# Performance work log

Hardware: AMD Instinct MI355X
Metric: run time of the kernel (lower is better)

The kernel has to match this reference:

```python
import jax, jax.numpy as jnp
import numpy as np

N, E = 50000, 1600000
H, C = 4, 32            # heads, out_channels per head (hidden_dim // heads)
HID, LAT = 128, 32
NEG_SLOPE = 0.2


def setup_inputs() -> dict:
    key = jax.random.key(0)
    ks = jax.random.split(key, 16)
    g = lambda k, shape, fan: jax.random.normal(k, shape, jnp.float32) * (1.0 / np.sqrt(fan))
    return {
        "x": jax.random.normal(ks[0], (N, 3), jnp.float32),
        "edge_index": jax.random.randint(ks[1], (2, E), 0, N, jnp.int64),
        "edge_attr": jax.random.normal(ks[2], (E, 7), jnp.float32),
        # GATConv params
        "W_gat": g(ks[3], (3, H * C), 3),          # lin (shared src/dst)
        "att_src": g(ks[4], (H, C), C),
        "att_dst": g(ks[5], (H, C), C),
        "W_edge": g(ks[6], (7, H * C), 7),         # lin_edge
        "att_edge": g(ks[7], (H, C), C),
        "bias_gat": jnp.zeros((H * C,), jnp.float32),
        # GCNEncoder MLP params
        "W1": g(ks[8], (HID, HID), HID),
        "b1": jnp.zeros((HID,), jnp.float32),
        "prelu_a": jnp.float32(0.25),
        "W2": g(ks[9], (HID, LAT), HID),
        "b2": jnp.zeros((LAT,), jnp.float32),
    }


def _gat_encoder(x, edge_index, edge_attr, W_gat, att_src, att_dst, W_edge,
                 att_edge, bias_gat, W1, b1, prelu_a, W2, b2):
    src, dst = edge_index[0], edge_index[1]
    n = x.shape[0]

    # add self-loops; self-loop edge_attr = mean of incoming edge_attr (PyG fill_value='mean')
    deg = jax.ops.segment_sum(jnp.ones_like(dst, jnp.float32), dst, num_segments=n)
    ea_mean = jax.ops.segment_sum(edge_attr, dst, num_segments=n) / jnp.clip(deg, 1.0)[:, None]
    loops = jnp.arange(n, dtype=src.dtype)
    src_f = jnp.concatenate([src, loops])
    dst_f = jnp.concatenate([dst, loops])
    ea_f = jnp.concatenate([edge_attr, ea_mean], axis=0)

    xp = (x @ W_gat).reshape(n, H, C)                      # [N,H,C]
    a_src = jnp.einsum('nhc,hc->nh', xp, att_src)          # [N,H]
    a_dst = jnp.einsum('nhc,hc->nh', xp, att_dst)
    ep = (ea_f @ W_edge).reshape(-1, H, C)                 # [E',H,C]
    a_edge = jnp.einsum('ehc,hc->eh', ep, att_edge)

    alpha = jax.nn.leaky_relu(a_src[src_f] + a_dst[dst_f] + a_edge, NEG_SLOPE)  # [E',H]
    m = jax.ops.segment_max(alpha, dst_f, num_segments=n)
    ealpha = jnp.exp(alpha - m[dst_f])
    denom = jax.ops.segment_sum(ealpha, dst_f, num_segments=n)
    alpha = ealpha / denom[dst_f]

    msg = xp[src_f] * alpha[:, :, None]                    # [E',H,C]
    out = jax.ops.segment_sum(msg, dst_f, num_segments=n)  # [N,H,C]
    h = jax.nn.elu(out.reshape(n, H * C) + bias_gat)

    h1 = h @ W1 + b1
    h1 = jnp.where(h1 > 0, h1, prelu_a * h1)               # PReLU
    return h1 @ W2 + b2


def reference(x, edge_index, edge_attr, W_gat, att_src, att_dst, W_edge,
              att_edge, bias_gat, W1, b1, prelu_a, W2, b2):
    return _gat_encoder(x, edge_index, edge_attr, W_gat, att_src, att_dst,
                        W_edge, att_edge, bias_gat, W1, b1, prelu_a, W2, b2)
```

## Files before the change

kernel.cpp:

```cpp
#include <hip/hip_runtime.h>
#include <cstdint>

#define N_NODES 50000
#define N_EDGES 1600000
#define NH 4
#define CC 32
#define HC 128
#define LAT 32
#define NEG_SLOPE 0.2f

#define NB_HIST 250
#define CH_E    6400
#define NB_NODE 25
#define NB_PRE  (NB_HIST + NB_NODE + 3)

#define NBUCK 196
#define P1_T  512
#define P1_EPB (P1_T * 4)
#define P1_BLOCKS ((N_EDGES + P1_EPB - 1) / P1_EPB)
#define CAP  8960

typedef uint32_t u32x4 __attribute__((ext_vector_type(4)));
typedef __bf16   bf16x8 __attribute__((ext_vector_type(8)));
typedef float    f32x4 __attribute__((ext_vector_type(4)));

__device__ __forceinline__ float bflo(uint32_t u) {
    union { uint32_t i; float f; } c; c.i = u << 16; return c.f;
}
__device__ __forceinline__ float bfhi(uint32_t u) {
    union { uint32_t i; float f; } c; c.i = u & 0xFFFF0000u; return c.f;
}
__device__ __forceinline__ uint32_t f2bf(float f) {
    union { float f; uint32_t i; } c; c.f = f;
    return (c.i + 0x7FFFu + ((c.i >> 16) & 1u)) >> 16;
}
__device__ __forceinline__ uint32_t pack2(float a, float b) {
    return f2bf(a) | (f2bf(b) << 16);
}
__device__ __forceinline__ float bpermf(int byteIdx, float v) {
    return __int_as_float(__builtin_amdgcn_ds_bpermute(byteIdx, __float_as_int(v)));
}
__device__ __forceinline__ uint32_t f2e4m3(float x) {
    uint32_t u = __float_as_uint(x);
    uint32_t s = u >> 31;
    uint32_t mag = u & 0x7fffffffu;
    mag += 0x7ffffu + ((mag >> 20) & 1u);
    uint32_t e = mag >> 23;
    if (e < 121u) return s << 7;
    uint32_t code = ((e - 120u) << 3) | ((mag >> 20) & 7u);
    if (code > 0x7Eu) code = 0x7Eu;
    return (s << 7) | code;
}
__device__ __forceinline__ float e4m32f(uint32_t b) {
    uint32_t e = (b >> 3) & 15u;
    if (e == 0u) return 0.f;
    return __uint_as_float(((b >> 7) << 31) | ((e + 120u) << 23) | ((b & 7u) << 20));
}


__global__ __launch_bounds__(256) void k_pre(const float* __restrict__ x,
                                             const int* __restrict__ ei,
                                             const float* __restrict__ W_gat,
                                             const float* __restrict__ att_src,
                                             const float* __restrict__ att_dst,
                                             const float* __restrict__ W_edge,
                                             const float* __restrict__ att_edge,
                                             const float* __restrict__ W1,
                                             const float* __restrict__ W2,
                                             uint16_t* __restrict__ hist,
                                             float4* __restrict__ a_src,
                                             float4* __restrict__ a_dst,
                                             float* __restrict__ v,
                                             uint16_t* __restrict__ W1T_hi,
                                             uint16_t* __restrict__ W1T_lo,
                                             uint16_t* __restrict__ W2T_hi,
                                             uint16_t* __restrict__ W2T_lo) {
    __shared__ uint32_t lh[12500];
    int bid = blockIdx.x, t = threadIdx.x;
    if (bid < NB_HIST) {
        int b = bid;
        int base = b * CH_E;
        uint32_t* orow = (uint32_t*)(hist + (size_t)b * N_NODES);
        #pragma unroll 1
        for (int p = 0; p < 2; ++p) {
            for (int i = t; i < 12500; i += 256) lh[i] = 0;
            __syncthreads();
            int lo = p * 25000;
            #pragma unroll 1
            for (int it = 0; it < CH_E / 256; ++it) {
                int dst = ei[N_EDGES + base + it * 256 + t];
                int r = dst - lo;
                if (r >= 0 && r < 25000)
                    atomicAdd(&lh[r >> 1], 1u << ((r & 1) * 16));
            }
            __syncthreads();
            for (int i = t; i < 12500; i += 256)
                orow[p * 12500 + i] = lh[i];
            __syncthreads();
        }
    } else if (bid < NB_HIST + NB_NODE) {
        __shared__ float us[12], ud[12];
        if (t < 12) {
            int i = t >> 2, h = t & 3;
            float s = 0.f;
            #pragma unroll
            for (int c = 0; c < 32; ++c)
                s += W_gat[i * 128 + h * 32 + c] * att_src[h * 32 + c];
            us[t] = s;
        } else if (t < 24) {
            int q = t - 12; int i = q >> 2, h = q & 3;
            float s = 0.f;
            #pragma unroll
            for (int c = 0; c < 32; ++c)
                s += W_gat[i * 128 + h * 32 + c] * att_dst[h * 32 + c];
            ud[q] = s;
        }
        __syncthreads();
        int base = (bid - NB_HIST) * 2048;
        #pragma unroll 1
        for (int i = 0; i < 8; ++i) {
            int n = base + i * 256 + t;
            if (n >= N_NODES) break;
            float x0 = x[n * 3 + 0], x1 = x[n * 3 + 1], x2 = x[n * 3 + 2];
            float s[4], d[4];
            #pragma unroll
            for (int h = 0; h < 4; ++h) {
                s[h] = x0 * us[h] + x1 * us[4 + h] + x2 * us[8 + h];
                d[h] = x0 * ud[h] + x1 * ud[4 + h] + x2 * ud[8 + h];
            }
            a_src[n] = make_float4(s[0], s[1], s[2], s[3]);
            a_dst[n] = make_float4(d[0], d[1], d[2], d[3]);
        }
    } else if (bid == NB_HIST + NB_NODE) {
        if (t < 28) {
            int d = t >> 2, h = t & 3;
            float s = 0.f;
            #pragma unroll
            for (int c = 0; c < 32; ++c)
                s += W_edge[d * 128 + h * 32 + c] * att_edge[h * 32 + c];
            v[t] = s;
        }
    } else if (bid == NB_HIST + NB_NODE + 1) {
        #pragma unroll 4
        for (int i = 0; i < 64; ++i) {
            int idx = i * 256 + t;
            int n = idx >> 7, k = idx & 127;
            float vv = W1[k * 128 + n];
            uint32_t hi = f2bf(vv);
            uint32_t lo = f2bf(vv - bflo(hi));
            W1T_hi[idx] = (uint16_t)hi;
            W1T_lo[idx] = (uint16_t)lo;
        }
    } else {
        #pragma unroll 4
        for (int i = 0; i < 16; ++i) {
            int idx = i * 256 + t;
            int j = idx >> 7, k = idx & 127;
            float vv = W2[k * 32 + j];
            uint32_t hi = f2bf(vv);
            uint32_t lo = f2bf(vv - bflo(hi));
            W2T_hi[idx] = (uint16_t)hi;
            W2T_lo[idx] = (uint16_t)lo;
        }
    }
}

__global__ __launch_bounds__(256) void k_red(const uint16_t* __restrict__ hist,
                                             int* __restrict__ cnt,
                                             int* __restrict__ bsum) {
    __shared__ int red[256];
    int t = threadIdx.x;
    int i = blockIdx.x * 256 + t;
    int run = 0;
    if (i < N_NODES) {
        int r[10];
        #pragma unroll
        for (int j = 0; j < 10; ++j) r[j] = 0;
        size_t off = i;
        #pragma unroll 1
        for (int b = 0; b < 25; ++b) {
            #pragma unroll
            for (int j = 0; j < 10; ++j)
                r[j] += hist[off + (size_t)j * N_NODES];
            off += (size_t)10 * N_NODES;
        }
        #pragma unroll
        for (int j = 1; j < 10; ++j) r[0] += r[j];
        run = r[0];
        cnt[i] = run;
    }
    red[t] = run;
    __syncthreads();
    #pragma unroll
    for (int s = 128; s > 0; s >>= 1) {
        if (t < s) red[t] += red[t + s];
        __syncthreads();
    }
    if (t == 0) bsum[blockIdx.x] = red[0];
}

__global__ __launch_bounds__(256) void k_scanb(const int* __restrict__ bsum,
                                               int* __restrict__ bbase) {
    __shared__ int sh[256];
    int t = threadIdx.x;
    int vv = (t < NBUCK) ? bsum[t] : 0;
    sh[t] = vv;
    __syncthreads();
    #pragma unroll
    for (int off = 1; off < 256; off <<= 1) {
        int xv = (t >= off) ? sh[t - off] : 0;
        __syncthreads();
        sh[t] += xv;
        __syncthreads();
    }
    if (t < NBUCK) bbase[t] = sh[t] - vv;
    if (t == 255) bbase[NBUCK] = sh[255];
}

__global__ __launch_bounds__(256) void k_local(const int* __restrict__ cnt,
                                               const int* __restrict__ bbase,
                                               int* __restrict__ rowptr,
                                               int* __restrict__ bcur) {
    __shared__ int sh[256];
    int b = blockIdx.x, t = threadIdx.x;
    int i = b * 256 + t;
    int vv = (i < N_NODES) ? cnt[i] : 0;
    sh[t] = vv;
    __syncthreads();
    #pragma unroll
    for (int off = 1; off < 256; off <<= 1) {
        int xv = (t >= off) ? sh[t - off] : 0;
        __syncthreads();
        sh[t] += xv;
        __syncthreads();
    }
    int base = bbase[b];
    if (i < N_NODES) rowptr[i] = base + sh[t] - vv;
    if (t == 0) bcur[b] = base;
    if (b == 0 && t == 0) rowptr[N_NODES] = bbase[NBUCK];
}

__global__ __launch_bounds__(512) void k_scat1(const int* __restrict__ ei,
                                               const float* __restrict__ edge_attr,
                                               const float* __restrict__ v,
                                               const float4* __restrict__ a_src,
                                               int* __restrict__ bcur,
                                               uint4* __restrict__ stg) {
    __shared__ int bh[NBUCK];
    __shared__ int bg[NBUCK];
    __shared__ int bl[NBUCK];
    __shared__ int bo[NBUCK];
    __shared__ int sct[256];
    __shared__ u32x4 lrec[P1_EPB];
    __shared__ int gaddr[P1_EPB];
    int t = threadIdx.x;
    float vsr[28];
    #pragma unroll
    for (int i = 0; i < 28; ++i) vsr[i] = v[i];

    for (int i = t; i < NBUCK; i += P1_T) bh[i] = 0;
    __syncthreads();

    int e0 = blockIdx.x * P1_EPB + t * 4;
    bool act = (e0 < N_EDGES);
    int dst[4];
    uint4 rec[4];
    if (act) {
        int4 s4 = *(const int4*)&ei[e0];
        int4 d4 = *(const int4*)&ei[N_EDGES + e0];
        int srcv[4] = {s4.x, s4.y, s4.z, s4.w};
        dst[0] = d4.x; dst[1] = d4.y; dst[2] = d4.z; dst[3] = d4.w;

        float4 as4[4];
        #pragma unroll
        for (int q = 0; q < 4; ++q)
            as4[q] = a_src[srcv[q]];

        const float4* ea4 = (const float4*)&edge_attr[e0 * 7];
        float ea[28];
        #pragma unroll
        for (int i = 0; i < 7; ++i) {
            float4 vv = ea4[i];
            ea[i * 4 + 0] = vv.x; ea[i * 4 + 1] = vv.y;
            ea[i * 4 + 2] = vv.z; ea[i * 4 + 3] = vv.w;
        }

        #pragma unroll
        for (int q = 0; q < 4; ++q) {
            float asv[4] = {as4[q].x, as4[q].y, as4[q].z, as4[q].w};
            float comb[4];
            uint32_t ae8 = 0;
            #pragma unroll
            for (int h = 0; h < 4; ++h) {
                float aeh = 0.f;
                #pragma unroll
                for (int d = 0; d < 7; ++d) aeh += ea[q * 7 + d] * vsr[d * 4 + h];
                ae8 |= f2e4m3(aeh) << (h * 8);
                comb[h] = aeh + asv[h];
            }
            rec[q] = make_uint4(pack2(comb[0], comb[1]), pack2(comb[2], comb[3]),
                                (uint32_t)srcv[q] | ((uint32_t)(dst[q] & 255) << 16),
                                ae8);
            atomicAdd(&bh[dst[q] >> 8], 1);
        }
    }
    __syncthreads();
    int hv = 0;
    if (t < 256) { hv = (t < NBUCK) ? bh[t] : 0; sct[t] = hv; }
    __syncthreads();
    #pragma unroll
    for (int off = 1; off < 256; off <<= 1) {
        int xv = 0;
        if (t < 256 && t >= off) xv = sct[t - off];
        __syncthreads();
        if (t < 256) sct[t] += xv;
        __syncthreads();
    }
    if (t < NBUCK) {
        bo[t] = sct[t] - hv;
        bg[t] = hv ? atomicAdd(&bcur[t], hv) : 0;
        bl[t] = 0;
    }
    __syncthreads();
    if (act) {
        #pragma unroll
        for (int q = 0; q < 4; ++q) {
            int bk = dst[q] >> 8;
            int off = atomicAdd(&bl[bk], 1);
            int slot = bo[bk] + off;
            lrec[slot] = (u32x4){rec[q].x, rec[q].y, rec[q].z, rec[q].w};
            gaddr[slot] = bg[bk] + off;
        }
    }
    __syncthreads();
    int total = sct[255];
    for (int s = t; s < total; s += P1_T) {
        u32x4 r = lrec[s];
        stg[gaddr[s]] = make_uint4(r.x, r.y, r.z, r.w);
    }
}

__global__ __launch_bounds__(1024) void k_scat2g(const int* __restrict__ rowptr,
                                                 const int* __restrict__ bbase,
                                                 const uint4* __restrict__ stg,
                                                 const float* __restrict__ x,
                                                 const float* __restrict__ a_src,
                                                 const float* __restrict__ a_dst,
                                                 const float* __restrict__ W_gat,
                                                 const float* __restrict__ bias_gat,
                                                 float2* __restrict__ h_buf) {
    __shared__ int rp[257];
    __shared__ int lcnt[256];
    __shared__ u32x4 lrec[CAP];
    int b = blockIdx.x, t = threadIdx.x;
    int n0 = b << 8;
    int nn = min(256, N_NODES - n0);
    int base = bbase[b];
    for (int i = t; i <= nn; i += 1024) rp[i] = rowptr[n0 + i] - base;
    __syncthreads();
    for (int i = t; i < nn; i += 1024) lcnt[i] = rp[i + 1] - rp[i];
    __syncthreads();
    int total = rp[nn];

    for (int e = t; e < total; e += 1024) {
        uint4 r = stg[base + e];
        int dl = (int)((r.z >> 16) & 0xFFu);
        int c = atomicSub(&lcnt[dl], 1);
        int slot = rp[dl] + c - 1;
        if (slot < CAP) lrec[slot] = (u32x4){r.x, r.y, r.z, r.w};
    }
    __syncthreads();

    int wv = t >> 6, l = t & 63;
    int h = l & 3;
    int slot = l >> 2;
    int c0 = 2 * l;
    float w00 = W_gat[c0],       w01 = W_gat[c0 + 1];
    float w10 = W_gat[128 + c0], w11 = W_gat[128 + c0 + 1];
    float w20 = W_gat[256 + c0], w21 = W_gat[256 + c0 + 1];
    float2 bia = ((const float2*)bias_gat)[l];

    #pragma unroll 1
    for (int j = 0; j < 16; ++j) {
        int i = wv * 16 + j;
        if (i >= nn) break;
        int n = n0 + i;
        int start = rp[i], end = rp[i + 1];
        int deg = end - start;
        float ad_n = a_dst[n * 4 + h];
        float as_n = a_src[n * 4 + h];
        float sx0 = 0.f, sx1 = 0.f, sx2 = 0.f, den = 0.f, aes = 0.f;

        for (int p0 = start; p0 < end; p0 += 16) {
            int e = p0 + slot;
            float w = 0.f, ae = 0.f;
            int src = n;
            if (e < end) {
                u32x4 rc = lrec[e];
                uint32_t aw = (h < 2) ? rc.x : rc.y;
                float comb = (h & 1) ? bfhi(aw) : bflo(aw);
                ae = e4m32f((rc.w >> (h * 8)) & 0xffu);
                src = (int)(rc.z & 0xFFFFu);
                float al = comb + ad_n;
                al = al > 0.f ? al : NEG_SLOPE * al;
                w = __expf(al);
            }
            const float* xr = x + src * 3;
            sx0 += w * xr[0];
            sx1 += w * xr[1];
            sx2 += w * xr[2];
            den += w;
            aes += ae;
        }

        #pragma unroll
        for (int m = 4; m <= 32; m <<= 1) {
            sx0 += __shfl_xor(sx0, m);
            sx1 += __shfl_xor(sx1, m);
            sx2 += __shfl_xor(sx2, m);
            den += __shfl_xor(den, m);
            aes += __shfl_xor(aes, m);
        }

        float xn0 = x[n * 3], xn1 = x[n * 3 + 1], xn2 = x[n * 3 + 2];
        float invd = (deg > 0) ? (1.0f / (float)deg) : 1.0f;
        float alS = as_n + ad_n + aes * invd;
        alS = alS > 0.f ? alS : NEG_SLOPE * alS;
        float wS = __expf(alS);
        sx0 += wS * xn0; sx1 += wS * xn1; sx2 += wS * xn2;
        den += wS;

        int sb = (l >> 4) << 2;
        float t0 = bpermf(sb, sx0);
        float t1 = bpermf(sb, sx1);
        float t2 = bpermf(sb, sx2);
        float td = bpermf(sb, den);

        float r = 1.0f / td;
        float o0 = (t0 * w00 + t1 * w10 + t2 * w20) * r + bia.x;
        float o1 = (t0 * w01 + t1 * w11 + t2 * w21) * r + bia.y;
        o0 = o0 > 0.f ? o0 : (__expf(o0) - 1.0f);
        o1 = o1 > 0.f ? o1 : (__expf(o1) - 1.0f);
        h_buf[(size_t)n * 64 + l] = make_float2(o0, o1);
    }
}

__global__ __launch_bounds__(256) void k_mlp(const float* __restrict__ h_buf,
                                             const uint16_t* __restrict__ W1T_hi,
                                             const uint16_t* __restrict__ W1T_lo,
                                             const uint16_t* __restrict__ W2T_hi,
                                             const uint16_t* __restrict__ W2T_lo,
                                             const float* __restrict__ b1,
                                             const float* __restrict__ prelu_a,
                                             const float* __restrict__ b2,
                                             float* __restrict__ out) {
    __shared__ uint16_t hHi[32 * 136];
    __shared__ uint16_t hLo[32 * 136];
    __shared__ uint16_t h1Hi[32 * 136];
    __shared__ uint16_t h1Lo[32 * 136];
    int t = threadIdx.x;
    int nb = blockIdx.x * 32;

    const float4* hb4 = (const float4*)(h_buf + (size_t)nb * 128);
    #pragma unroll
    for (int i = 0; i < 4; ++i) {
        int idx = i * 256 + t;
        int row = idx >> 5, c4 = idx & 31;
        float4 v = make_float4(0.f, 0.f, 0.f, 0.f);
        if (nb + row < N_NODES) v = hb4[idx];
        float xs[4] = {v.x, v.y, v.z, v.w};
        uint32_t hi[4], lo[4];
        #pragma unroll
        for (int j = 0; j < 4; ++j) {
            hi[j] = f2bf(xs[j]);
            lo[j] = f2bf(xs[j] - bflo(hi[j]));
        }
        uint32_t bo = row * 272 + c4 * 8;
        *(uint2*)((char*)hHi + bo) = make_uint2(hi[0] | (hi[1] << 16), hi[2] | (hi[3] << 16));
        *(uint2*)((char*)hLo + bo) = make_uint2(lo[0] | (lo[1] << 16), lo[2] | (lo[3] << 16));
    }
    __syncthreads();

    int w = t >> 6, l = t & 63;
    int lr = l & 15, lg = l >> 4;
    float bb0 = b1[(2 * w) * 16 + lr];
    float bb1 = b1[(2 * w + 1) * 16 + lr];
    f32x4 acc[2][2];
    #pragma unroll
    for (int rt = 0; rt < 2; ++rt) {
        acc[rt][0] = (f32x4){bb0, bb0, bb0, bb0};
        acc[rt][1] = (f32x4){bb1, bb1, bb1, bb1};
    }
    #pragma unroll
    for (int s = 0; s < 4; ++s) {
        int koff = s * 64 + lg * 16;
        bf16x8 a_hi[2], a_lo[2], b_hi[2], b_lo[2];
        #pragma unroll
        for (int rt = 0; rt < 2; ++rt) {
            int ro = (rt * 16 + lr) * 272 + koff;
            a_hi[rt] = *(const bf16x8*)((const char*)hHi + ro);
            a_lo[rt] = *(const bf16x8*)((const char*)hLo + ro);
        }
        #pragma unroll
        for (int c = 0; c < 2; ++c) {
            int go = ((2 * w + c) * 16 + lr) * 256 + koff;
            b_hi[c] = *(const bf16x8*)((const char*)W1T_hi + go);
            b_lo[c] = *(const bf16x8*)((const char*)W1T_lo + go);
        }
        #pragma unroll
        for (int rt = 0; rt < 2; ++rt)
            #pragma unroll
            for (int c = 0; c < 2; ++c) {
                acc[rt][c] = __builtin_amdgcn_mfma_f32_16x16x32_bf16(a_hi[rt], b_hi[c], acc[rt][c], 0, 0, 0);
                acc[rt][c] = __builtin_amdgcn_mfma_f32_16x16x32_bf16(a_hi[rt], b_lo[c], acc[rt][c], 0, 0, 0);
                acc[rt][c] = __builtin_amdgcn_mfma_f32_16x16x32_bf16(a_lo[rt], b_hi[c], acc[rt][c], 0, 0, 0);
            }
    }
    float pa = prelu_a[0];
    #pragma unroll
    for (int rt = 0; rt < 2; ++rt)
        #pragma unroll
        for (int c = 0; c < 2; ++c) {
            int n = (2 * w + c) * 16 + lr;
            #pragma unroll
            for (int r = 0; r < 4; ++r) {
                float vv = acc[rt][c][r];
                vv = vv > 0.f ? vv : pa * vv;
                uint32_t hi = f2bf(vv);
                uint32_t lo = f2bf(vv - bflo(hi));
                int m = rt * 16 + lg * 4 + r;
                uint32_t bo = m * 272 + n * 2;
                *(uint16_t*)((char*)h1Hi + bo) = (uint16_t)hi;
                *(uint16_t*)((char*)h1Lo + bo) = (uint16_t)lo;
            }
        }
    __syncthreads();
    int rt2 = w & 1, ct2 = w >> 1;
    float bb2 = b2[ct2 * 16 + lr];
    f32x4 acc2 = (f32x4){bb2, bb2, bb2, bb2};
    #pragma unroll
    for (int s = 0; s < 4; ++s) {
        int koff = s * 64 + lg * 16;
        int ro = (rt2 * 16 + lr) * 272 + koff;
        bf16x8 a_hi = *(const bf16x8*)((const char*)h1Hi + ro);
        bf16x8 a_lo = *(const bf16x8*)((const char*)h1Lo + ro);
        int go = (ct2 * 16 + lr) * 256 + koff;
        bf16x8 w2h = *(const bf16x8*)((const char*)W2T_hi + go);
        bf16x8 w2l = *(const bf16x8*)((const char*)W2T_lo + go);
        acc2 = __builtin_amdgcn_mfma_f32_16x16x32_bf16(a_hi, w2h, acc2, 0, 0, 0);
        acc2 = __builtin_amdgcn_mfma_f32_16x16x32_bf16(a_hi, w2l, acc2, 0, 0, 0);
        acc2 = __builtin_amdgcn_mfma_f32_16x16x32_bf16(a_lo, w2h, acc2, 0, 0, 0);
    }
    #pragma unroll
    for (int r = 0; r < 4; ++r) {
        int m = rt2 * 16 + lg * 4 + r;
        if (nb + m < N_NODES)
            out[(size_t)(nb + m) * 32 + ct2 * 16 + lr] = acc2[r];
    }
}


extern "C" void kernel_launch(void* const* d_in, const int* in_sizes, int n_in,
                              void* d_out, int out_size, void* d_ws, size_t ws_size,
                              hipStream_t stream) {
    const float* x        = (const float*)d_in[0];
    const int*   ei       = (const int*)d_in[1];
    const float* edge_attr= (const float*)d_in[2];
    const float* W_gat    = (const float*)d_in[3];
    const float* att_src  = (const float*)d_in[4];
    const float* att_dst  = (const float*)d_in[5];
    const float* W_edge   = (const float*)d_in[6];
    const float* att_edge = (const float*)d_in[7];
    const float* bias_gat = (const float*)d_in[8];
    const float* W1       = (const float*)d_in[9];
    const float* b1       = (const float*)d_in[10];
    const float* prelu_a  = (const float*)d_in[11];
    const float* W2       = (const float*)d_in[12];
    const float* b2       = (const float*)d_in[13];
    float*       out      = (float*)d_out;

    char* base = (char*)d_ws;
    size_t off = 0;
    auto alloc = [&](size_t bytes) -> void* {
        void* p = base + off;
        off = (off + bytes + 255) & ~(size_t)255;
        return p;
    };
    int*      cnt     = (int*)     alloc((size_t)N_NODES * 4);
    int*      rowptr  = (int*)     alloc((size_t)(N_NODES + 1) * 4);
    int*      bcur    = (int*)     alloc((size_t)NBUCK * 4);
    int*      bsum    = (int*)     alloc((size_t)NBUCK * 4);
    int*      bbase   = (int*)     alloc((size_t)(NBUCK + 1) * 4);
    float*    v       = (float*)   alloc(32 * 4);
    uint16_t* W1T_hi  = (uint16_t*)alloc((size_t)128 * 128 * 2);
    uint16_t* W1T_lo  = (uint16_t*)alloc((size_t)128 * 128 * 2);
    uint16_t* W2T_hi  = (uint16_t*)alloc((size_t)32 * 128 * 2);
    uint16_t* W2T_lo  = (uint16_t*)alloc((size_t)32 * 128 * 2);
    float*    a_src   = (float*)   alloc((size_t)N_NODES * 4 * 4);
    float*    a_dst   = (float*)   alloc((size_t)N_NODES * 4 * 4);
    float*    h_buf   = (float*)   alloc((size_t)N_NODES * 128 * 4);
    size_t stg_bytes  = (size_t)N_EDGES * 16;
    size_t hist_bytes = (size_t)NB_HIST * N_NODES * 2;
    void* stg_region  = alloc(stg_bytes > hist_bytes ? stg_bytes : hist_bytes);
    uint16_t* hist    = (uint16_t*)stg_region;
    uint4*    stg     = (uint4*)stg_region;

    k_pre   <<<NB_PRE, 256, 0, stream>>>(x, ei, W_gat, att_src, att_dst,
                                         W_edge, att_edge, W1, W2, hist,
                                         (float4*)a_src, (float4*)a_dst, v,
                                         W1T_hi, W1T_lo, W2T_hi, W2T_lo);
    k_red   <<<NBUCK, 256, 0, stream>>>(hist, cnt, bsum);
    k_scanb <<<1, 256, 0, stream>>>(bsum, bbase);
    k_local <<<NBUCK, 256, 0, stream>>>(cnt, bbase, rowptr, bcur);
    k_scat1 <<<P1_BLOCKS, P1_T, 0, stream>>>(
        ei, edge_attr, v, (const float4*)a_src, bcur, stg);
    k_scat2g<<<NBUCK, 1024, 0, stream>>>(
        rowptr, bbase, stg, x, a_src, a_dst, W_gat, bias_gat, (float2*)h_buf);
    k_mlp   <<<(N_NODES + 31) / 32, 256, 0, stream>>>(
        h_buf, W1T_hi, W1T_lo, W2T_hi, W2T_lo, b1, prelu_a, b2, out);
}
```

Before: 243.8 us.

## Replace per-block LDS histograms with global atomic degree counting

Degree counting previously built per-block shared-memory histograms (packed 16-bit counters over two passes), wrote 250 partial rows to global memory, and reduced them in a separate kernel. Now each edge does a global atomicAdd into a zeroed count array, and the reduce kernel only computes block sums. This removes the large partial-histogram write and read (about 25 MB) and the two-pass LDS work. In exchange it adds 1.6M contended global atomics and an extra zeroing kernel launch.

```diff
diff --git a/kernel.cpp b/kernel.cpp
--- a/kernel.cpp
+++ b/kernel.cpp
@@ -9,10 +9,10 @@
 #define LAT 32
 #define NEG_SLOPE 0.2f
 
-#define NB_HIST 250
+#define NB_CNT  250
 #define CH_E    6400
 #define NB_NODE 25
-#define NB_PRE  (NB_HIST + NB_NODE + 3)
+#define NB_PRE  (NB_CNT + NB_NODE + 3)
 
 #define NBUCK 196
 #define P1_T  512
@@ -58,6 +58,11 @@
 }
 
 
+__global__ __launch_bounds__(1024) void k_zero(int* __restrict__ cnt) {
+    int i = blockIdx.x * 1024 + threadIdx.x;
+    if (i < N_NODES) cnt[i] = 0;
+}
+
 __global__ __launch_bounds__(256) void k_pre(const float* __restrict__ x,
                                              const int* __restrict__ ei,
                                              const float* __restrict__ W_gat,
@@ -67,7 +72,7 @@
                                              const float* __restrict__ att_edge,
                                              const float* __restrict__ W1,
                                              const float* __restrict__ W2,
-                                             uint16_t* __restrict__ hist,
+                                             int* __restrict__ cnt,
                                              float4* __restrict__ a_src,
                                              float4* __restrict__ a_dst,
                                              float* __restrict__ v,
@@ -75,30 +80,15 @@
                                              uint16_t* __restrict__ W1T_lo,
                                              uint16_t* __restrict__ W2T_hi,
                                              uint16_t* __restrict__ W2T_lo) {
-    __shared__ uint32_t lh[12500];
     int bid = blockIdx.x, t = threadIdx.x;
-    if (bid < NB_HIST) {
-        int b = bid;
-        int base = b * CH_E;
-        uint32_t* orow = (uint32_t*)(hist + (size_t)b * N_NODES);
+    if (bid < NB_CNT) {
+        int base = bid * CH_E;
         #pragma unroll 1
-        for (int p = 0; p < 2; ++p) {
-            for (int i = t; i < 12500; i += 256) lh[i] = 0;
-            __syncthreads();
-            int lo = p * 25000;
-            #pragma unroll 1
-            for (int it = 0; it < CH_E / 256; ++it) {
-                int dst = ei[N_EDGES + base + it * 256 + t];
-                int r = dst - lo;
-                if (r >= 0 && r < 25000)
-                    atomicAdd(&lh[r >> 1], 1u << ((r & 1) * 16));
-            }
-            __syncthreads();
-            for (int i = t; i < 12500; i += 256)
-                orow[p * 12500 + i] = lh[i];
-            __syncthreads();
-        }
-    } else if (bid < NB_HIST + NB_NODE) {
+        for (int it = 0; it < CH_E / 256; ++it) {
+            int dst = ei[N_EDGES + base + it * 256 + t];
+            atomicAdd(&cnt[dst], 1);
+        }
+    } else if (bid < NB_CNT + NB_NODE) {
         __shared__ float us[12], ud[12];
         if (t < 12) {
             int i = t >> 2, h = t & 3;
@@ -116,7 +106,7 @@
             ud[q] = s;
         }
         __syncthreads();
-        int base = (bid - NB_HIST) * 2048;
+        int base = (bid - NB_CNT) * 2048;
         #pragma unroll 1
         for (int i = 0; i < 8; ++i) {
             int n = base + i * 256 + t;
@@ -131,7 +121,7 @@
             a_src[n] = make_float4(s[0], s[1], s[2], s[3]);
             a_dst[n] = make_float4(d[0], d[1], d[2], d[3]);
         }
-    } else if (bid == NB_HIST + NB_NODE) {
+    } else if (bid == NB_CNT + NB_NODE) {
         if (t < 28) {
             int d = t >> 2, h = t & 3;
             float s = 0.f;
@@ -140,7 +130,7 @@
                 s += W_edge[d * 128 + h * 32 + c] * att_edge[h * 32 + c];
             v[t] = s;
         }
-    } else if (bid == NB_HIST + NB_NODE + 1) {
+    } else if (bid == NB_CNT + NB_NODE + 1) {
         #pragma unroll 4
         for (int i = 0; i < 64; ++i) {
             int idx = i * 256 + t;
@@ -165,31 +155,12 @@
     }
 }
 
-__global__ __launch_bounds__(256) void k_red(const uint16_t* __restrict__ hist,
-                                             int* __restrict__ cnt,
-                                             int* __restrict__ bsum) {
+__global__ __launch_bounds__(256) void k_bsum(const int* __restrict__ cnt,
+                                              int* __restrict__ bsum) {
     __shared__ int red[256];
     int t = threadIdx.x;
     int i = blockIdx.x * 256 + t;
-    int run = 0;
-    if (i < N_NODES) {
-        int r[10];
-        #pragma unroll
-        for (int j = 0; j < 10; ++j) r[j] = 0;
-        size_t off = i;
-        #pragma unroll 1
-        for (int b = 0; b < 25; ++b) {
-            #pragma unroll
-            for (int j = 0; j < 10; ++j)
-                r[j] += hist[off + (size_t)j * N_NODES];
-            off += (size_t)10 * N_NODES;
-        }
-        #pragma unroll
-        for (int j = 1; j < 10; ++j) r[0] += r[j];
-        run = r[0];
-        cnt[i] = run;
-    }
-    red[t] = run;
+    red[t] = (i < N_NODES) ? cnt[i] : 0;
     __syncthreads();
     #pragma unroll
     for (int s = 128; s > 0; s >>= 1) {
@@ -599,17 +570,14 @@
     float*    a_src   = (float*)   alloc((size_t)N_NODES * 4 * 4);
     float*    a_dst   = (float*)   alloc((size_t)N_NODES * 4 * 4);
     float*    h_buf   = (float*)   alloc((size_t)N_NODES * 128 * 4);
-    size_t stg_bytes  = (size_t)N_EDGES * 16;
-    size_t hist_bytes = (size_t)NB_HIST * N_NODES * 2;
-    void* stg_region  = alloc(stg_bytes > hist_bytes ? stg_bytes : hist_bytes);
-    uint16_t* hist    = (uint16_t*)stg_region;
-    uint4*    stg     = (uint4*)stg_region;
-
+    uint4*    stg     = (uint4*)   alloc((size_t)N_EDGES * 16);
+
+    k_zero  <<<(N_NODES + 1023) / 1024, 1024, 0, stream>>>(cnt);
     k_pre   <<<NB_PRE, 256, 0, stream>>>(x, ei, W_gat, att_src, att_dst,
-                                         W_edge, att_edge, W1, W2, hist,
+                                         W_edge, att_edge, W1, W2, cnt,
                                          (float4*)a_src, (float4*)a_dst, v,
                                          W1T_hi, W1T_lo, W2T_hi, W2T_lo);
-    k_red   <<<NBUCK, 256, 0, stream>>>(hist, cnt, bsum);
+    k_bsum  <<<NBUCK, 256, 0, stream>>>(cnt, bsum);
     k_scanb <<<1, 256, 0, stream>>>(bsum, bbase);
     k_local <<<NBUCK, 256, 0, stream>>>(cnt, bbase, rowptr, bcur);
     k_scat1 <<<P1_BLOCKS, P1_T, 0, stream>>>(
```

New measurement: 277.6 us. 1.14x slower.
